# Performance work log

Measured on AMD Instinct MI355X. Metric: run time of the kernel, lower is better.

Reference implementation:

```python
import jax, jax.numpy as jnp
import numpy as np
import math

T, R, H, DK = 3, 4, 8, 32   # num_types, num_relations, n_heads, d_k
OUT = H * DK                # out_dim = 256
IN = 256                    # in_dim (== out_dim, required by residual)
B, N = 4, 1024              # batch, max_nodes
LN_EPS = 1e-5


def setup_inputs() -> dict:
    key = jax.random.key(0)
    ks = jax.random.split(key, 12)
    a = math.sqrt(6.0 / (2 * DK))  # xavier_uniform bound for [d_k,d_k]
    w = 0.02
    return {
        "node_features":   jax.random.normal(ks[0], (B, N, IN), jnp.float32),
        "node_types_soft": jax.random.uniform(ks[1], (B, N, T), jnp.float32),
        "adj_matrix_soft": jax.random.uniform(ks[2], (B, N, N), jnp.float32),
        "edge_types_soft": jax.random.uniform(ks[3], (B, N, N, R), jnp.float32),
        "Wq": jax.random.normal(ks[4], (T, IN, OUT), jnp.float32) * w,
        "bq": jnp.zeros((T, OUT), jnp.float32),
        "Wk": jax.random.normal(ks[5], (T, IN, OUT), jnp.float32) * w,
        "bk": jnp.zeros((T, OUT), jnp.float32),
        "Wv": jax.random.normal(ks[6], (T, IN, OUT), jnp.float32) * w,
        "bv": jnp.zeros((T, OUT), jnp.float32),
        "Wa": jax.random.normal(ks[7], (T, OUT, OUT), jnp.float32) * w,
        "ba": jnp.zeros((T, OUT), jnp.float32),
        "rel_pri": jnp.ones((R, H), jnp.float32),
        "rel_att": jax.random.uniform(ks[8], (R, H, DK, DK), jnp.float32, -a, a),
        "rel_msg": jax.random.uniform(ks[9], (R, H, DK, DK), jnp.float32, -a, a),
        "skip": jnp.ones((T,), jnp.float32),
        "ln_gamma": jnp.ones((T, OUT), jnp.float32),
        "ln_beta": jnp.zeros((T, OUT), jnp.float32),
    }


def _single(x, types, adj, erel, Wq, bq, Wk, bk, Wv, bv, Wa, ba,
            rel_pri, rel_att, rel_msg, skip, ln_gamma, ln_beta):
    # x:[N,in], types:[N,T], adj:[N,N], erel:[N,N,R]
    n = x.shape[0]
    sqrt_dk = float(np.sqrt(DK))
    # per-type projections -> [T,N,H,DK]
    Qt = (jnp.einsum('nd,tdo->tno', x, Wq) + bq[:, None, :]).reshape(T, n, H, DK)
    Kt = (jnp.einsum('nd,tdo->tno', x, Wk) + bk[:, None, :]).reshape(T, n, H, DK)
    Vt = (jnp.einsum('nd,tdo->tno', x, Wv) + bv[:, None, :]).reshape(T, n, H, DK)
    # relation-transformed K/V: [T,R,N,H,DK]
    Ksr = jnp.einsum('tnhd,rhde->trnhe', Kt, rel_att)
    Vsr = jnp.einsum('tnhd,rhde->trnhe', Vt, rel_msg)
    # soft-type mixtures (sums over target/source types factor out of the mask)
    Qbar = jnp.einsum('nt,tnhd->nhd', types, Qt)            # target mix
    Kbar = jnp.einsum('nt,trnhd->rnhd', types, Ksr)         # source mix, per relation
    # accumulated (masked, unnormalized) attention logits [N,N,H]
    res_att = jnp.zeros((n, n, H), x.dtype)
    for r in range(R):
        coef = (adj * erel[:, :, r])[:, :, None] * (rel_pri[r] / sqrt_dk)  # [N,N,H]
        res_att = res_att + coef * jnp.einsum('ihd,jhd->ijh', Qbar, Kbar[r])
    # per-target-row softmax over sources (dim j), zeroed if row-sum tiny
    row_sum = res_att.sum(axis=(1, 2))                       # [N]
    attn = jnp.where((row_sum > 1e-6)[:, None, None],
                     jax.nn.softmax(res_att, axis=1), 0.0)
    # aggregated = sum_{s,r,j} attn * masked score * V_{s,r}  (never builds [N,N,H,DK])
    agg = jnp.zeros((n, H, DK), x.dtype)
    for r in range(R):
        coef = (adj * erel[:, :, r])[:, :, None] * (rel_pri[r] / sqrt_dk)
        for s in range(T):
            score = coef * types[None, :, s, None] * jnp.einsum('ihd,jhd->ijh', Qbar, Ksr[s, r])
            agg = agg + jnp.einsum('ijh,ijh,jhd->ihd', attn, score, Vsr[s, r])
    agg = agg.reshape(n, OUT)
    # per-type output head: a_linear(gelu(agg)), gated residual, layernorm, soft-type mix
    g = jax.nn.gelu(agg, approximate=False)
    trans = jnp.einsum('no,tod->tnd', g, Wa) + ba[:, None, :]          # [T,N,OUT]
    alpha = jax.nn.sigmoid(skip)[:, None, None]
    res = trans * alpha + x[None] * (1.0 - alpha)
    mu = res.mean(axis=-1, keepdims=True)
    var = ((res - mu) ** 2).mean(axis=-1, keepdims=True)
    ln = (res - mu) / jnp.sqrt(var + LN_EPS) * ln_gamma[:, None, :] + ln_beta[:, None, :]
    return jnp.einsum('nt,tnd->nd', types, ln)


def reference(node_features, node_types_soft, adj_matrix_soft, edge_types_soft,
              Wq, bq, Wk, bk, Wv, bv, Wa, ba, rel_pri, rel_att, rel_msg,
              skip, ln_gamma, ln_beta):
    f = jax.vmap(_single, in_axes=(0, 0, 0, 0) + (None,) * 14)
    return f(node_features, node_types_soft, adj_matrix_soft, edge_types_soft,
             Wq, bq, Wk, bk, Wv, bv, Wa, ba, rel_pri, rel_att, rel_msg,
             skip, ln_gamma, ln_beta)
```

## Files before the change

kernel.cpp:

```cpp
#include <hip/hip_runtime.h>
#include <math.h>

constexpr int CB = 4, CN = 1024, CT = 3, CR = 4, CH = 8, CDK = 32, COUT = 256;

typedef __attribute__((ext_vector_type(4))) float f32x4;
typedef __attribute__((ext_vector_type(8))) short s16x8;
typedef __attribute__((ext_vector_type(4))) _Float16 f16x4;
typedef __attribute__((ext_vector_type(8))) _Float16 f16x8;
typedef __attribute__((ext_vector_type(4))) unsigned short u16x4;
typedef __attribute__((ext_vector_type(8))) unsigned short u16x8;

__device__ inline unsigned short f2bf(float x) {
    unsigned u = __float_as_uint(x);
    unsigned r = (u + 0x7fffu + ((u >> 16) & 1u)) >> 16;
    return (unsigned short)r;
}
__device__ inline float bf2f(unsigned short b) {
    return __uint_as_float(((unsigned)b) << 16);
}

__global__ void zero_rs(float* __restrict__ rs) {
    rs[blockIdx.x * 256 + threadIdx.x] = 0.f;
}

__global__ void splitx(const float* __restrict__ X,
                       unsigned short* __restrict__ Xh, unsigned short* __restrict__ Xl)
{
    size_t idx = ((size_t)blockIdx.x * 256 + threadIdx.x) * 4;
    f32x4 v = *(const f32x4*)(X + idx);
    u16x4 hv, lv;
    #pragma unroll
    for (int k = 0; k < 4; ++k) {
        unsigned short hb = f2bf(v[k]);
        hv[k] = hb;
        lv[k] = f2bf(v[k] - bf2f(hb));
    }
    *(u16x4*)(Xh + idx) = hv;
    *(u16x4*)(Xl + idx) = lv;
}

__global__ __launch_bounds__(256) void wsplit(
    const float* __restrict__ Wq, const float* __restrict__ Wk,
    const float* __restrict__ Wv, const float* __restrict__ Wa,
    unsigned short* __restrict__ WTh, unsigned short* __restrict__ WTl)
{
    int z = blockIdx.z;
    int t = z % 3;
    const float* W;
    if (z < 9) { int w3 = z / 3; W = (w3 == 0 ? Wq : (w3 == 1 ? Wk : Wv)); }
    else W = Wa;
    W += (size_t)t * COUT * COUT;
    int k0 = blockIdx.x * 32, n0 = blockIdx.y * 32;
    __shared__ float tl[32][33];
    int tid = threadIdx.x;
    {
        int k = tid >> 3, n4 = (tid & 7) * 4;
        f32x4 v = *(const f32x4*)(W + (size_t)(k0 + k) * COUT + n0 + n4);
        tl[n4 + 0][k] = v[0]; tl[n4 + 1][k] = v[1];
        tl[n4 + 2][k] = v[2]; tl[n4 + 3][k] = v[3];
    }
    __syncthreads();
    int n = tid >> 3, k4 = (tid & 7) * 4;
    u16x4 hv, lv;
    #pragma unroll
    for (int j = 0; j < 4; ++j) {
        float x = tl[n][k4 + j];
        unsigned short hb = f2bf(x);
        hv[j] = hb; lv[j] = f2bf(x - bf2f(hb));
    }
    size_t off = (size_t)z * COUT * COUT + (size_t)(n0 + n) * COUT + k0 + k4;
    *(u16x4*)(WTh + off) = hv;
    *(u16x4*)(WTl + off) = lv;
}

__global__ __launch_bounds__(256) void mfma_gemm(
    int mode,
    const unsigned short* __restrict__ Ah, const unsigned short* __restrict__ Al,
    const unsigned short* __restrict__ WTh, const unsigned short* __restrict__ WTl,
    const float* __restrict__ bq, const float* __restrict__ bk,
    const float* __restrict__ bv, const float* __restrict__ ba,
    float* __restrict__ Y0, float* __restrict__ Y1, float* __restrict__ Y2)
{
    int z = blockIdx.z;
    int b, t, widx;
    const float* bias;
    float* Y;
    if (mode == 0) {
        b = z / 9; int r9 = z % 9; int w3 = r9 / 3; t = r9 % 3;
        widx = w3 * 3 + t;
        bias = (w3 == 0 ? bq : (w3 == 1 ? bk : bv)) + t * COUT;
        Y = (w3 == 0 ? Y0 : (w3 == 1 ? Y1 : Y2)) + ((size_t)b * CT + t) * CN * COUT;
    } else {
        b = z / CT; t = z % CT;
        widx = 9 + t;
        bias = ba + t * COUT;
        Y = Y0 + ((size_t)b * CT + t) * CN * COUT;
    }
    const unsigned short* Ahb = Ah + (size_t)b * CN * COUT;
    const unsigned short* Alb = Al + (size_t)b * CN * COUT;
    const unsigned short* Bhb = WTh + (size_t)widx * COUT * COUT;
    const unsigned short* Blb = WTl + (size_t)widx * COUT * COUT;

    const int M0 = blockIdx.x * 128, N0 = blockIdx.y * 128;
    __shared__ unsigned short As[2][128][40];
    __shared__ unsigned short Bs[2][128][40];
    const int tid = threadIdx.x;
    const int wave = tid >> 6, lane = tid & 63;
    const int wm = wave & 1, wn = wave >> 1;
    const int col = lane & 15, quad = lane >> 4;

    f32x4 acc[4][4];
    #pragma unroll
    for (int mt = 0; mt < 4; ++mt)
        #pragma unroll
        for (int nt = 0; nt < 4; ++nt) acc[mt][nt] = (f32x4){0.f, 0.f, 0.f, 0.f};

    for (int kt = 0; kt < COUT; kt += 32) {
        #pragma unroll
        for (int q = 0; q < 2; ++q) {
            int f = q * 256 + tid;
            int m = f >> 2, kc = (f & 3) * 8;
            *(u16x8*)&As[0][m][kc] = *(const u16x8*)(Ahb + (size_t)(M0 + m) * COUT + kt + kc);
            *(u16x8*)&As[1][m][kc] = *(const u16x8*)(Alb + (size_t)(M0 + m) * COUT + kt + kc);
            *(u16x8*)&Bs[0][m][kc] = *(const u16x8*)(Bhb + (size_t)(N0 + m) * COUT + kt + kc);
            *(u16x8*)&Bs[1][m][kc] = *(const u16x8*)(Blb + (size_t)(N0 + m) * COUT + kt + kc);
        }
        __syncthreads();
        s16x8 ah[4], al4[4], bh[4], bl4[4];
        #pragma unroll
        for (int mt = 0; mt < 4; ++mt) {
            ah[mt]  = *(const s16x8*)&As[0][wm * 64 + mt * 16 + col][quad * 8];
            al4[mt] = *(const s16x8*)&As[1][wm * 64 + mt * 16 + col][quad * 8];
        }
        #pragma unroll
        for (int nt = 0; nt < 4; ++nt) {
            bh[nt]  = *(const s16x8*)&Bs[0][wn * 64 + nt * 16 + col][quad * 8];
            bl4[nt] = *(const s16x8*)&Bs[1][wn * 64 + nt * 16 + col][quad * 8];
        }
        #pragma unroll
        for (int mt = 0; mt < 4; ++mt)
            #pragma unroll
            for (int nt = 0; nt < 4; ++nt) {
                acc[mt][nt] = __builtin_amdgcn_mfma_f32_16x16x32_bf16(al4[mt], bh[nt], acc[mt][nt], 0, 0, 0);
                acc[mt][nt] = __builtin_amdgcn_mfma_f32_16x16x32_bf16(ah[mt], bl4[nt], acc[mt][nt], 0, 0, 0);
                acc[mt][nt] = __builtin_amdgcn_mfma_f32_16x16x32_bf16(ah[mt], bh[nt], acc[mt][nt], 0, 0, 0);
            }
        __syncthreads();
    }
    float bb[4];
    #pragma unroll
    for (int nt = 0; nt < 4; ++nt) bb[nt] = bias[N0 + wn * 64 + nt * 16 + col];
    #pragma unroll
    for (int mt = 0; mt < 4; ++mt)
        #pragma unroll
        for (int nt = 0; nt < 4; ++nt) {
            int n = N0 + wn * 64 + nt * 16 + col;
            #pragma unroll
            for (int reg = 0; reg < 4; ++reg) {
                int m = M0 + wm * 64 + mt * 16 + quad * 4 + reg;
                Y[(size_t)m * COUT + n] = acc[mt][nt][reg] + bb[nt];
            }
        }
}

__global__ void mix_qbar(const float* __restrict__ Qt, const float* __restrict__ types,
                         float* __restrict__ Qbar)
{
    int idx = blockIdx.x * 256 + threadIdx.x;
    int bi = idx >> 6;
    int o4 = (idx & 63) * 4;
    int b = bi >> 10;
    const float* tp = types + (size_t)bi * CT;
    float t0 = tp[0], t1 = tp[1], t2 = tp[2];
    size_t nbase = ((size_t)b * CT) * CN * COUT + (size_t)(bi & 1023) * COUT + o4;
    float4 q0 = *(const float4*)(Qt + nbase);
    float4 q1 = *(const float4*)(Qt + nbase + (size_t)CN * COUT);
    float4 q2 = *(const float4*)(Qt + nbase + 2 * (size_t)CN * COUT);
    float4 o;
    o.x = t0 * q0.x + t1 * q1.x + t2 * q2.x;
    o.y = t0 * q0.y + t1 * q1.y + t2 * q2.y;
    o.z = t0 * q0.z + t1 * q1.z + t2 * q2.z;
    o.w = t0 * q0.w + t1 * q1.w + t2 * q2.w;
    *(float4*)(Qbar + (size_t)bi * COUT + o4) = o;
}

__global__ __launch_bounds__(256) void qr3_kernel(const float* __restrict__ Qbar,
                                                  const float* __restrict__ rel_att,
                                                  const float* __restrict__ rel_pri,
                                                  unsigned short* __restrict__ Qrhi,
                                                  unsigned short* __restrict__ Qrlo)
{
    int i0 = blockIdx.x * 8;
    int rh = blockIdx.y; int r = rh >> 3, h = rh & 7;
    int b = blockIdx.z;
    __shared__ float A_s[32][33];
    __shared__ float q_s[8][32];
    int tid = threadIdx.x;
    {
        int f = tid * 4; int d = f >> 5, e = f & 31;
        float4 v = *(const float4*)(rel_att + ((size_t)rh * 32 + d) * 32 + e);
        A_s[d][e] = v.x; A_s[d][e + 1] = v.y; A_s[d][e + 2] = v.z; A_s[d][e + 3] = v.w;
        int ii = tid >> 5, ee = tid & 31;
        q_s[ii][ee] = Qbar[((size_t)b * CN + i0 + ii) * COUT + h * CDK + ee];
    }
    __syncthreads();
    int d = tid & 31, ii = tid >> 5;
    float acc = 0.f;
    #pragma unroll 8
    for (int e = 0; e < 32; ++e) acc += A_s[d][e] * q_s[ii][e];
    const float inv_sqrt = 0.17677669529663687f;
    float v = acc * rel_pri[rh] * inv_sqrt;
    unsigned short hb = f2bf(v);
    float lo = v - bf2f(hb);
    size_t oidx = ((((size_t)b * CR + r) * CH + h) * CN + i0 + ii) * CDK + d;
    Qrhi[oidx] = hb;
    Qrlo[oidx] = f2bf(lo);
}

__global__ __launch_bounds__(256) void prep_k(const float* __restrict__ Kt,
                                              const float* __restrict__ types,
                                              unsigned short* __restrict__ Kbh,
                                              unsigned short* __restrict__ Kbl,
                                              unsigned short* __restrict__ Kty)
{
    int b = blockIdx.y;
    int j = blockIdx.x * 8 + (threadIdx.x >> 5);
    int c = threadIdx.x & 31;
    int h = c >> 2, d0 = (c & 3) * 8;
    const float* tp = types + ((size_t)b * CN + j) * CT;
    float kb[8];
    #pragma unroll
    for (int k = 0; k < 8; ++k) kb[k] = 0.f;
    #pragma unroll
    for (int s = 0; s < 3; ++s) {
        float ty = tp[s];
        const float* src = Kt + (((size_t)(b * 3 + s)) * CN + j) * COUT + c * 8;
        f32x4 a0 = *(const f32x4*)(src);
        f32x4 a1 = *(const f32x4*)(src + 4);
        u16x8 kt8;
        #pragma unroll
        for (int k = 0; k < 4; ++k) {
            float v0 = ty * a0[k], v1 = ty * a1[k];
            kt8[k] = f2bf(v0); kt8[4 + k] = f2bf(v1);
            kb[k] += v0; kb[4 + k] += v1;
        }
        *(u16x8*)(Kty + (((size_t)(b * 3 + s) * CH + h) * CN + j) * CDK + d0) = kt8;
    }
    u16x8 hv, lv;
    #pragma unroll
    for (int k = 0; k < 8; ++k) {
        unsigned short hb = f2bf(kb[k]);
        hv[k] = hb; lv[k] = f2bf(kb[k] - bf2f(hb));
    }
    *(u16x8*)(Kbh + (((size_t)b * CH + h) * CN + j) * CDK + d0) = hv;
    *(u16x8*)(Kbl + (((size_t)b * CH + h) * CN + j) * CDK + d0) = lv;
}

__global__ __launch_bounds__(256) void vT_kernel(const float* __restrict__ Vt,
                                                 _Float16* __restrict__ VT)
{
    int j0 = blockIdx.x * 64; int h = blockIdx.y; int bs = blockIdx.z;
    __shared__ float tile[32][72];
    int t = threadIdx.x;
    int jj = t >> 2, e8 = (t & 3) * 8;
    const float* src = Vt + ((size_t)bs * CN + j0 + jj) * COUT + h * CDK + e8;
    f32x4 v0 = *(const f32x4*)(src);
    f32x4 v1 = *(const f32x4*)(src + 4);
    #pragma unroll
    for (int k = 0; k < 4; ++k) { tile[e8 + k][jj] = v0[k]; tile[e8 + 4 + k][jj] = v1[k]; }
    __syncthreads();
    int e = t >> 3, jr = (t & 7) * 8;
    f16x8 o;
    #pragma unroll
    for (int k = 0; k < 8; ++k) o[k] = (_Float16)tile[e][jr + k];
    *(f16x8*)(VT + (((size_t)bs * CH + h) * CDK + e) * CN + j0 + jr) = o;
}

__global__ void mT_kernel(const float* __restrict__ rel_msg, _Float16* __restrict__ MT)
{
    int rh = blockIdx.x; int t = threadIdx.x;
    int e = t >> 3, ep4 = (t & 7) * 4;
    f16x4 o;
    #pragma unroll
    for (int k = 0; k < 4; ++k)
        o[k] = (_Float16)rel_msg[((size_t)rh * 32 + ep4 + k) * 32 + e];
    *(f16x4*)(MT + ((size_t)rh * 32 + e) * 32 + ep4) = o;
}

__global__ __launch_bounds__(256) void coef_t(const float* __restrict__ adj,
                                              const float* __restrict__ erel,
                                              float* __restrict__ coefT)
{
    int b = blockIdx.z; int i0 = blockIdx.y * 32; int j0 = blockIdx.x * 32;
    __shared__ float tile[32][132];
    int t = threadIdx.x;
    {
        int ii = t >> 3, jc = t & 7;
        size_t arow = ((size_t)b * CN + i0 + ii) * CN + j0;
        f32x4 av = *(const f32x4*)(adj + arow + jc * 4);
        #pragma unroll
        for (int kk = 0; kk < 4; ++kk) {
            int j = jc * 4 + kk;
            f32x4 ev = *(const f32x4*)(erel + (arow + j) * 4);
            float a = av[kk];
            f32x4 cv;
            cv[0] = ev[0] * a; cv[1] = ev[1] * a; cv[2] = ev[2] * a; cv[3] = ev[3] * a;
            *(f32x4*)&tile[j][ii * 4] = cv;
        }
    }
    __syncthreads();
    {
        int jj = t >> 3, ic = t & 7;
        size_t orow = ((size_t)b * CN + j0 + jj) * CN + i0;
        #pragma unroll
        for (int kk = 0; kk < 4; ++kk)
            *(f32x4*)(coefT + (orow + ic * 4 + kk) * 4) = *(const f32x4*)&tile[jj][(ic * 4 + kk) * 4];
    }
}

__global__ __launch_bounds__(256, 3) void attn3_kernel(
    const unsigned short* __restrict__ Qrhi, const unsigned short* __restrict__ Qrlo,
    const unsigned short* __restrict__ Kbh,  const unsigned short* __restrict__ Kbl,
    const unsigned short* __restrict__ Kty,
    const _Float16* __restrict__ VT,
    const float* __restrict__ coefT,
    float* __restrict__ Upart,
    float* __restrict__ lbuf,
    float* __restrict__ rowsum)
{
    const int h = blockIdx.y;
    const int z = blockIdx.z; const int b = z >> 1, part = z & 1;
    const int tid = threadIdx.x;
    const int wave = tid >> 6, lane = tid & 63;
    const int col = lane & 15, quad = lane >> 4;
    const int i = blockIdx.x * 64 + wave * 16 + col;
    const int jbase = part * 512;

    __shared__ _Float16 vs[2][3][32][20];

    s16x8 qh[4], ql[4];
    #pragma unroll
    for (int r = 0; r < 4; ++r) {
        size_t off = ((((size_t)b * CR + r) * CH + h) * CN + i) * CDK + quad * 8;
        qh[r] = *(const s16x8*)(Qrhi + off);
        ql[r] = *(const s16x8*)(Qrlo + off);
    }

    const int e_st = tid >> 3, jc_st = tid & 7;
    size_t vtb[3];
    #pragma unroll
    for (int s = 0; s < 3; ++s)
        vtb[s] = (((size_t)(b * 3 + s) * CH + h) * CDK + e_st) * CN + jc_st * 2;

    #pragma unroll
    for (int s = 0; s < 3; ++s)
        *(unsigned*)&vs[0][s][e_st][jc_st * 2] = *(const unsigned*)(VT + vtb[s] + jbase);
    __syncthreads();

    f32x4 U[4][2];
    #pragma unroll
    for (int r = 0; r < 4; ++r) { U[r][0] = (f32x4){0.f,0.f,0.f,0.f}; U[r][1] = (f32x4){0.f,0.f,0.f,0.f}; }
    float lpart = 0.f, rspart = 0.f;

    const size_t kbbase = (((size_t)b * CH + h) * CN + col) * CDK + quad * 8;
    size_t ktbase[3];
    #pragma unroll
    for (int s = 0; s < 3; ++s)
        ktbase[s] = (((size_t)(b * 3 + s) * CH + h) * CN + col) * CDK + quad * 8;

    #pragma unroll 1
    for (int js = 0; js < 32; ++js) {
        const int j0 = jbase + js * 16;
        const int buf = js & 1;
        const int jn = jbase + ((js + 1 < 32) ? (js + 1) * 16 : js * 16);
        unsigned pf0 = *(const unsigned*)(VT + vtb[0] + jn);
        unsigned pf1 = *(const unsigned*)(VT + vtb[1] + jn);
        unsigned pf2 = *(const unsigned*)(VT + vtb[2] + jn);

        s16x8 kbh_ = *(const s16x8*)(Kbh + kbbase + (size_t)j0 * CDK);
        s16x8 kbl_ = *(const s16x8*)(Kbl + kbbase + (size_t)j0 * CDK);
        s16x8 kt[3];
        #pragma unroll
        for (int s = 0; s < 3; ++s)
            kt[s] = *(const s16x8*)(Kty + ktbase[s] + (size_t)j0 * CDK);
        f32x4 cf[4];
        #pragma unroll
        for (int reg = 0; reg < 4; ++reg)
            cf[reg] = *(const f32x4*)(coefT + (((size_t)b * CN + j0 + quad * 4 + reg) * CN + i) * 4);

        f32x4 Db[4];
        #pragma unroll
        for (int r = 0; r < 4; ++r) {
            f32x4 d = {0.f, 0.f, 0.f, 0.f};
            d = __builtin_amdgcn_mfma_f32_16x16x32_bf16(kbl_, qh[r], d, 0, 0, 0);
            d = __builtin_amdgcn_mfma_f32_16x16x32_bf16(kbh_, ql[r], d, 0, 0, 0);
            d = __builtin_amdgcn_mfma_f32_16x16x32_bf16(kbh_, qh[r], d, 0, 0, 0);
            Db[r] = d;
        }
        float P[4];
        #pragma unroll
        for (int reg = 0; reg < 4; ++reg) {
            float L = cf[reg][0] * Db[0][reg] + cf[reg][1] * Db[1][reg]
                    + cf[reg][2] * Db[2][reg] + cf[reg][3] * Db[3][reg];
            rspart += L;
            P[reg] = __expf(L);
            lpart += P[reg];
        }
        #pragma unroll
        for (int s = 0; s < 3; ++s) {
            f32x4 Dp[4];
            #pragma unroll
            for (int r = 0; r < 4; ++r) {
                f32x4 d = {0.f, 0.f, 0.f, 0.f};
                Dp[r] = __builtin_amdgcn_mfma_f32_16x16x32_bf16(kt[s], qh[r], d, 0, 0, 0);
            }
            f16x4 v0 = *(const f16x4*)&vs[buf][s][col][quad * 4];
            f16x4 v1 = *(const f16x4*)&vs[buf][s][col + 16][quad * 4];
            #pragma unroll
            for (int r = 0; r < 4; ++r) {
                f16x4 w;
                w[0] = (_Float16)(P[0] * cf[0][r] * Dp[r][0]);
                w[1] = (_Float16)(P[1] * cf[1][r] * Dp[r][1]);
                w[2] = (_Float16)(P[2] * cf[2][r] * Dp[r][2]);
                w[3] = (_Float16)(P[3] * cf[3][r] * Dp[r][3]);
                U[r][0] = __builtin_amdgcn_mfma_f32_16x16x16f16(v0, w, U[r][0], 0, 0, 0);
                U[r][1] = __builtin_amdgcn_mfma_f32_16x16x16f16(v1, w, U[r][1], 0, 0, 0);
            }
        }
        *(unsigned*)&vs[buf ^ 1][0][e_st][jc_st * 2] = pf0;
        *(unsigned*)&vs[buf ^ 1][1][e_st][jc_st * 2] = pf1;
        *(unsigned*)&vs[buf ^ 1][2][e_st][jc_st * 2] = pf2;
        __syncthreads();
    }

    float l = lpart;  l += __shfl_xor(l, 16);  l += __shfl_xor(l, 32);
    float rv = rspart; rv += __shfl_xor(rv, 16); rv += __shfl_xor(rv, 32);
    if (quad == 0) {
        lbuf[(((size_t)part * CB + b) * CH + h) * CN + i] = l;
        atomicAdd(rowsum + (size_t)b * CN + i, rv);
    }
    int itile = blockIdx.x * 4 + wave;
    size_t ub = ((((size_t)(b * CH + h) * 64 + itile) * 2 + part)) * 2048;
    #pragma unroll
    for (int r = 0; r < 4; ++r)
        #pragma unroll
        for (int eh = 0; eh < 2; ++eh)
            *(f32x4*)(Upart + ub + (size_t)(r * 2 + eh) * 256 + lane * 4) = U[r][eh];
}

__global__ __launch_bounds__(256) void merge_gelu(
    const float* __restrict__ Upart, const float* __restrict__ lbuf,
    const _Float16* __restrict__ MT, const float* __restrict__ rowsum,
    unsigned short* __restrict__ Gh, unsigned short* __restrict__ Gl)
{
    const int h = blockIdx.y, b = blockIdx.z;
    const int tid = threadIdx.x;
    const int wave = tid >> 6, lane = tid & 63;
    const int col = lane & 15, quad = lane >> 4;
    const int itile = blockIdx.x * 4 + wave;
    const int i = itile * 16 + col;

    size_t ub = ((size_t)(b * CH + h) * 64 + itile) * 2 * 2048;
    f32x4 U[4][2];
    #pragma unroll
    for (int r = 0; r < 4; ++r)
        #pragma unroll
        for (int eh = 0; eh < 2; ++eh) {
            f32x4 a = *(const f32x4*)(Upart + ub + (size_t)(r * 2 + eh) * 256 + lane * 4);
            f32x4 c = *(const f32x4*)(Upart + ub + 2048 + (size_t)(r * 2 + eh) * 256 + lane * 4);
            U[r][eh] = a + c;
        }
    float l = lbuf[(((size_t)0 * CB + b) * CH + h) * CN + i]
            + lbuf[(((size_t)1 * CB + b) * CH + h) * CN + i];
    float il = 1.f / l;
    f16x4 Uh[4][2];
    #pragma unroll
    for (int r = 0; r < 4; ++r)
        #pragma unroll
        for (int eh = 0; eh < 2; ++eh) {
            Uh[r][eh][0] = (_Float16)(U[r][eh][0] * il);
            Uh[r][eh][1] = (_Float16)(U[r][eh][1] * il);
            Uh[r][eh][2] = (_Float16)(U[r][eh][2] * il);
            Uh[r][eh][3] = (_Float16)(U[r][eh][3] * il);
        }
    float rsv = rowsum[(size_t)b * CN + i];
    bool gate = rsv > 1e-6f;
    const float is2 = 0.70710678118654752f;
    #pragma unroll
    for (int eo = 0; eo < 2; ++eo) {
        f32x4 acc = {0.f, 0.f, 0.f, 0.f};
        #pragma unroll
        for (int r = 0; r < 4; ++r)
            #pragma unroll
            for (int ep = 0; ep < 2; ++ep) {
                f16x4 mt = *(const f16x4*)(MT + ((size_t)(r * 8 + h) * 32 + eo * 16 + col) * 32
                                               + ep * 16 + quad * 4);
                acc = __builtin_amdgcn_mfma_f32_16x16x16f16(mt, Uh[r][ep], acc, 0, 0, 0);
            }
        u16x4 hv, lv;
        #pragma unroll
        for (int k = 0; k < 4; ++k) {
            float x = gate ? acc[k] : 0.f;
            float g = 0.5f * x * (1.f + erff(x * is2));
            unsigned short hb = f2bf(g);
            hv[k] = hb; lv[k] = f2bf(g - bf2f(hb));
        }
        size_t off = ((size_t)b * CN + i) * COUT + h * CDK + eo * 16 + quad * 4;
        *(u16x4*)(Gh + off) = hv;
        *(u16x4*)(Gl + off) = lv;
    }
}

__global__ __launch_bounds__(256) void final_ln2(
    const float* __restrict__ trans, const float* __restrict__ x,
    const float* __restrict__ types, const float* __restrict__ skip,
    const float* __restrict__ gamma, const float* __restrict__ beta,
    float* __restrict__ out)
{
    int wave = threadIdx.x >> 6, lane = threadIdx.x & 63;
    int bi = blockIdx.x * 4 + wave;
    int b = bi >> 10, i = bi & 1023;
    f32x4 xo = *(const f32x4*)(x + (size_t)bi * COUT + lane * 4);
    f32x4 accum = {0.f, 0.f, 0.f, 0.f};
    const float* tp = types + (size_t)bi * CT;
    #pragma unroll 1
    for (int t = 0; t < CT; ++t) {
        float al = 1.f / (1.f + __expf(-skip[t]));
        f32x4 tr = *(const f32x4*)(trans + (((size_t)b * CT + t) * CN + i) * COUT + lane * 4);
        f32x4 res;
        float s = 0.f;
        #pragma unroll
        for (int k = 0; k < 4; ++k) { res[k] = tr[k] * al + xo[k] * (1.f - al); s += res[k]; }
        #pragma unroll
        for (int mk = 1; mk < 64; mk <<= 1) s += __shfl_xor(s, mk);
        float mu = s * (1.f / COUT);
        f32x4 dc; float s2 = 0.f;
        #pragma unroll
        for (int k = 0; k < 4; ++k) { dc[k] = res[k] - mu; s2 += dc[k] * dc[k]; }
        #pragma unroll
        for (int mk = 1; mk < 64; mk <<= 1) s2 += __shfl_xor(s2, mk);
        float inv = rsqrtf(s2 * (1.f / COUT) + 1e-5f);
        f32x4 g = *(const f32x4*)(gamma + (size_t)t * COUT + lane * 4);
        f32x4 be = *(const f32x4*)(beta + (size_t)t * COUT + lane * 4);
        float ty = tp[t];
        #pragma unroll
        for (int k = 0; k < 4; ++k) accum[k] += ty * (dc[k] * inv * g[k] + be[k]);
    }
    *(f32x4*)(out + (size_t)bi * COUT + lane * 4) = accum;
}

extern "C" void kernel_launch(void* const* d_in, const int* in_sizes, int n_in,
                              void* d_out, int out_size, void* d_ws, size_t ws_size,
                              hipStream_t stream)
{
    (void)in_sizes; (void)n_in; (void)out_size; (void)ws_size;
    const float* nf      = (const float*)d_in[0];
    const float* types   = (const float*)d_in[1];
    const float* adj     = (const float*)d_in[2];
    const float* erel    = (const float*)d_in[3];
    const float* Wq      = (const float*)d_in[4];
    const float* bq      = (const float*)d_in[5];
    const float* Wk      = (const float*)d_in[6];
    const float* bk      = (const float*)d_in[7];
    const float* Wv      = (const float*)d_in[8];
    const float* bv      = (const float*)d_in[9];
    const float* Wa      = (const float*)d_in[10];
    const float* ba      = (const float*)d_in[11];
    const float* rel_pri = (const float*)d_in[12];
    const float* rel_att = (const float*)d_in[13];
    const float* rel_msg = (const float*)d_in[14];
    const float* skip    = (const float*)d_in[15];
    const float* gamma   = (const float*)d_in[16];
    const float* beta    = (const float*)d_in[17];
    float* out = (float*)d_out;

    float* ws = (float*)d_ws;
    size_t o = 0;
    float* pool0 = ws + o; o += 3 * (size_t)CB * CT * CN * COUT;
    float* Qt  = pool0;
    float* Ktb = pool0 + (size_t)CB * CT * CN * COUT;
    float* Vtb = pool0 + 2 * (size_t)CB * CT * CN * COUT;
    float* Qbar = ws + o; o += (size_t)CB * CN * COUT;
    float* rsb  = ws + o; o += (size_t)CB * CN;
    float* lbufp = ws + o; o += 2 * (size_t)CB * CH * CN;
    unsigned short* Qrhi = (unsigned short*)(ws + o); o += (size_t)CB * CR * CN * COUT / 2;
    unsigned short* Qrlo = (unsigned short*)(ws + o); o += (size_t)CB * CR * CN * COUT / 2;
    unsigned short* Kbh  = (unsigned short*)(ws + o); o += (size_t)CB * CH * CN * CDK / 2;
    unsigned short* Kbl  = (unsigned short*)(ws + o); o += (size_t)CB * CH * CN * CDK / 2;
    unsigned short* Kty  = (unsigned short*)(ws + o); o += (size_t)CB * CT * CH * CN * CDK / 2;
    _Float16* VTb = (_Float16*)(ws + o);              o += (size_t)CB * CT * CH * CDK * CN / 2;
    _Float16* MTb = (_Float16*)(ws + o);              o += (size_t)CR * CH * CDK * CDK / 2;
    unsigned short* Xh = (unsigned short*)(ws + o);   o += (size_t)CB * CN * COUT / 2;
    unsigned short* Xl = (unsigned short*)(ws + o);   o += (size_t)CB * CN * COUT / 2;
    unsigned short* Gh = (unsigned short*)(ws + o);   o += (size_t)CB * CN * COUT / 2;
    unsigned short* Gl = (unsigned short*)(ws + o);   o += (size_t)CB * CN * COUT / 2;
    unsigned short* WTh = (unsigned short*)(ws + o);  o += (size_t)12 * COUT * COUT / 2;
    unsigned short* WTl = (unsigned short*)(ws + o);  o += (size_t)12 * COUT * COUT / 2;
    float* coefT = ws + o; o += (size_t)CB * CN * CN * CR;
    float* Upart  = pool0;
    float* transb = pool0 + 3 * (size_t)CB * CN * COUT;

    zero_rs<<<CB * CN / 256, 256, 0, stream>>>(rsb);
    splitx<<<CB * CN * COUT / 4 / 256, 256, 0, stream>>>(nf, Xh, Xl);
    wsplit<<<dim3(8, 8, 12), 256, 0, stream>>>(Wq, Wk, Wv, Wa, WTh, WTl);
    mfma_gemm<<<dim3(8, 2, CB * 9), 256, 0, stream>>>(0, Xh, Xl, WTh, WTl,
                                                      bq, bk, bv, ba, Qt, Ktb, Vtb);
    coef_t<<<dim3(32, 32, CB), 256, 0, stream>>>(adj, erel, coefT);
    mix_qbar<<<CB * CN * COUT / 4 / 256, 256, 0, stream>>>(Qt, types, Qbar);
    qr3_kernel<<<dim3(CN / 8, CR * CH, CB), 256, 0, stream>>>(Qbar, rel_att, rel_pri, Qrhi, Qrlo);
    prep_k<<<dim3(CN / 8, CB), 256, 0, stream>>>(Ktb, types, Kbh, Kbl, Kty);
    vT_kernel<<<dim3(CN / 64, CH, CB * CT), 256, 0, stream>>>(Vtb, VTb);
    mT_kernel<<<CR * CH, 256, 0, stream>>>(rel_msg, MTb);
    attn3_kernel<<<dim3(16, CH, CB * 2), 256, 0, stream>>>(Qrhi, Qrlo, Kbh, Kbl, Kty, VTb, coefT,
                                                           Upart, lbufp, rsb);
    merge_gelu<<<dim3(16, CH, CB), 256, 0, stream>>>(Upart, lbufp, MTb, rsb, Gh, Gl);
    mfma_gemm<<<dim3(8, 2, CB * CT), 256, 0, stream>>>(1, Gh, Gl, WTh, WTl,
                                                       bq, bk, bv, ba, transb, transb, transb);
    final_ln2<<<CB * CN / 4, 256, 0, stream>>>(transb, nf, types, skip, gamma, beta, out);
}
```

Measured before the change: 383.1 us.

## Merge prep kernels into fewer launches and prefetch K/coef in attention loop

Result: faster. 374.7 us (-2.2%).

```diff
diff --git a/kernel.cpp b/kernel.cpp
--- a/kernel.cpp
+++ b/kernel.cpp
@@ -5,11 +5,14 @@
 
 typedef __attribute__((ext_vector_type(4))) float f32x4;
 typedef __attribute__((ext_vector_type(8))) short s16x8;
+typedef __attribute__((ext_vector_type(2))) _Float16 f16x2;
 typedef __attribute__((ext_vector_type(4))) _Float16 f16x4;
 typedef __attribute__((ext_vector_type(8))) _Float16 f16x8;
 typedef __attribute__((ext_vector_type(4))) unsigned short u16x4;
 typedef __attribute__((ext_vector_type(8))) unsigned short u16x8;
 
+union W4 { f16x4 v4; f16x2 v2[2]; };
+
 __device__ inline unsigned short f2bf(float x) {
     unsigned u = __float_as_uint(x);
     unsigned r = (u + 0x7fffu + ((u >> 16) & 1u)) >> 16;
@@ -18,59 +21,102 @@
 __device__ inline float bf2f(unsigned short b) {
     return __uint_as_float(((unsigned)b) << 16);
 }
-
-__global__ void zero_rs(float* __restrict__ rs) {
-    rs[blockIdx.x * 256 + threadIdx.x] = 0.f;
-}
-
-__global__ void splitx(const float* __restrict__ X,
-                       unsigned short* __restrict__ Xh, unsigned short* __restrict__ Xl)
-{
-    size_t idx = ((size_t)blockIdx.x * 256 + threadIdx.x) * 4;
-    f32x4 v = *(const f32x4*)(X + idx);
-    u16x4 hv, lv;
-    #pragma unroll
-    for (int k = 0; k < 4; ++k) {
-        unsigned short hb = f2bf(v[k]);
-        hv[k] = hb;
-        lv[k] = f2bf(v[k] - bf2f(hb));
-    }
-    *(u16x4*)(Xh + idx) = hv;
-    *(u16x4*)(Xl + idx) = lv;
-}
-
-__global__ __launch_bounds__(256) void wsplit(
+__device__ inline f16x2 pk2(float a, float b) {
+    auto t = __builtin_amdgcn_cvt_pkrtz(a, b);
+    f16x2 r;
+    __builtin_memcpy(&r, &t, sizeof(r));
+    return r;
+}
+
+__global__ __launch_bounds__(256) void prep0(
+    const float* __restrict__ nf,
+    unsigned short* __restrict__ Xh, unsigned short* __restrict__ Xl,
     const float* __restrict__ Wq, const float* __restrict__ Wk,
     const float* __restrict__ Wv, const float* __restrict__ Wa,
-    unsigned short* __restrict__ WTh, unsigned short* __restrict__ WTl)
-{
-    int z = blockIdx.z;
-    int t = z % 3;
-    const float* W;
-    if (z < 9) { int w3 = z / 3; W = (w3 == 0 ? Wq : (w3 == 1 ? Wk : Wv)); }
-    else W = Wa;
-    W += (size_t)t * COUT * COUT;
-    int k0 = blockIdx.x * 32, n0 = blockIdx.y * 32;
-    __shared__ float tl[32][33];
-    int tid = threadIdx.x;
-    {
-        int k = tid >> 3, n4 = (tid & 7) * 4;
-        f32x4 v = *(const f32x4*)(W + (size_t)(k0 + k) * COUT + n0 + n4);
-        tl[n4 + 0][k] = v[0]; tl[n4 + 1][k] = v[1];
-        tl[n4 + 2][k] = v[2]; tl[n4 + 3][k] = v[3];
-    }
-    __syncthreads();
-    int n = tid >> 3, k4 = (tid & 7) * 4;
-    u16x4 hv, lv;
-    #pragma unroll
-    for (int j = 0; j < 4; ++j) {
-        float x = tl[n][k4 + j];
-        unsigned short hb = f2bf(x);
-        hv[j] = hb; lv[j] = f2bf(x - bf2f(hb));
-    }
-    size_t off = (size_t)z * COUT * COUT + (size_t)(n0 + n) * COUT + k0 + k4;
-    *(u16x4*)(WTh + off) = hv;
-    *(u16x4*)(WTl + off) = lv;
+    unsigned short* __restrict__ WTh, unsigned short* __restrict__ WTl,
+    const float* __restrict__ rel_msg, _Float16* __restrict__ MT,
+    float* __restrict__ rs,
+    const float* __restrict__ adj, const float* __restrict__ erel,
+    float* __restrict__ coefT)
+{
+    __shared__ float smem[32 * 132];
+    const int bx = blockIdx.x, tid = threadIdx.x;
+    if (bx < 1024) {
+        size_t idx = ((size_t)bx * 256 + tid) * 4;
+        f32x4 v = *(const f32x4*)(nf + idx);
+        u16x4 hv, lv;
+        #pragma unroll
+        for (int k = 0; k < 4; ++k) {
+            unsigned short hb = f2bf(v[k]);
+            hv[k] = hb; lv[k] = f2bf(v[k] - bf2f(hb));
+        }
+        *(u16x4*)(Xh + idx) = hv;
+        *(u16x4*)(Xl + idx) = lv;
+    } else if (bx < 1792) {
+        int w = bx - 1024;
+        int zz = w >> 6; int rem = w & 63;
+        int k0 = (rem >> 3) * 32, n0 = (rem & 7) * 32;
+        int t = zz % 3;
+        const float* W;
+        if (zz < 9) { int w3 = zz / 3; W = (w3 == 0 ? Wq : (w3 == 1 ? Wk : Wv)); }
+        else W = Wa;
+        W += (size_t)t * COUT * COUT;
+        {
+            int k = tid >> 3, n4 = (tid & 7) * 4;
+            f32x4 v = *(const f32x4*)(W + (size_t)(k0 + k) * COUT + n0 + n4);
+            smem[(n4 + 0) * 33 + k] = v[0]; smem[(n4 + 1) * 33 + k] = v[1];
+            smem[(n4 + 2) * 33 + k] = v[2]; smem[(n4 + 3) * 33 + k] = v[3];
+        }
+        __syncthreads();
+        int n = tid >> 3, k4 = (tid & 7) * 4;
+        u16x4 hv, lv;
+        #pragma unroll
+        for (int j = 0; j < 4; ++j) {
+            float x = smem[n * 33 + k4 + j];
+            unsigned short hb = f2bf(x);
+            hv[j] = hb; lv[j] = f2bf(x - bf2f(hb));
+        }
+        size_t off = (size_t)zz * COUT * COUT + (size_t)(n0 + n) * COUT + k0 + k4;
+        *(u16x4*)(WTh + off) = hv;
+        *(u16x4*)(WTl + off) = lv;
+    } else if (bx < 1824) {
+        int rh = bx - 1792;
+        int e = tid >> 3, ep4 = (tid & 7) * 4;
+        f16x4 o;
+        #pragma unroll
+        for (int k = 0; k < 4; ++k)
+            o[k] = (_Float16)rel_msg[((size_t)rh * 32 + ep4 + k) * 32 + e];
+        *(f16x4*)(MT + ((size_t)rh * 32 + e) * 32 + ep4) = o;
+    } else if (bx < 1840) {
+        rs[(bx - 1824) * 256 + tid] = 0.f;
+    } else {
+        int c = bx - 1840;
+        int b = c >> 10; int rem = c & 1023;
+        int i0 = (rem >> 5) * 32; int j0 = (rem & 31) * 32;
+        {
+            int ii = tid >> 3, jc = tid & 7;
+            size_t arow = ((size_t)b * CN + i0 + ii) * CN + j0;
+            f32x4 av = *(const f32x4*)(adj + arow + jc * 4);
+            #pragma unroll
+            for (int kk = 0; kk < 4; ++kk) {
+                int j = jc * 4 + kk;
+                f32x4 ev = *(const f32x4*)(erel + (arow + j) * 4);
+                float a = av[kk];
+                f32x4 cv;
+                cv[0] = ev[0] * a; cv[1] = ev[1] * a; cv[2] = ev[2] * a; cv[3] = ev[3] * a;
+                *(f32x4*)&smem[j * 132 + ii * 4] = cv;
+            }
+        }
+        __syncthreads();
+        {
+            int jj = tid >> 3, ic = tid & 7;
+            size_t orow = ((size_t)b * CN + j0 + jj) * CN + i0;
+            #pragma unroll
+            for (int kk = 0; kk < 4; ++kk)
+                *(f32x4*)(coefT + (orow + ic * 4 + kk) * 4) =
+                    *(const f32x4*)&smem[jj * 132 + (ic * 4 + kk) * 4];
+        }
+    }
 }
 
 __global__ __launch_bounds__(256) void mfma_gemm(
@@ -217,116 +263,72 @@
     Qrlo[oidx] = f2bf(lo);
 }
 
-__global__ __launch_bounds__(256) void prep_k(const float* __restrict__ Kt,
-                                              const float* __restrict__ types,
-                                              unsigned short* __restrict__ Kbh,
-                                              unsigned short* __restrict__ Kbl,
-                                              unsigned short* __restrict__ Kty)
-{
-    int b = blockIdx.y;
-    int j = blockIdx.x * 8 + (threadIdx.x >> 5);
-    int c = threadIdx.x & 31;
-    int h = c >> 2, d0 = (c & 3) * 8;
-    const float* tp = types + ((size_t)b * CN + j) * CT;
-    float kb[8];
-    #pragma unroll
-    for (int k = 0; k < 8; ++k) kb[k] = 0.f;
-    #pragma unroll
-    for (int s = 0; s < 3; ++s) {
-        float ty = tp[s];
-        const float* src = Kt + (((size_t)(b * 3 + s)) * CN + j) * COUT + c * 8;
-        f32x4 a0 = *(const f32x4*)(src);
-        f32x4 a1 = *(const f32x4*)(src + 4);
-        u16x8 kt8;
-        #pragma unroll
-        for (int k = 0; k < 4; ++k) {
-            float v0 = ty * a0[k], v1 = ty * a1[k];
-            kt8[k] = f2bf(v0); kt8[4 + k] = f2bf(v1);
-            kb[k] += v0; kb[4 + k] += v1;
-        }
-        *(u16x8*)(Kty + (((size_t)(b * 3 + s) * CH + h) * CN + j) * CDK + d0) = kt8;
-    }
-    u16x8 hv, lv;
-    #pragma unroll
-    for (int k = 0; k < 8; ++k) {
-        unsigned short hb = f2bf(kb[k]);
-        hv[k] = hb; lv[k] = f2bf(kb[k] - bf2f(hb));
-    }
-    *(u16x8*)(Kbh + (((size_t)b * CH + h) * CN + j) * CDK + d0) = hv;
-    *(u16x8*)(Kbl + (((size_t)b * CH + h) * CN + j) * CDK + d0) = lv;
-}
-
-__global__ __launch_bounds__(256) void vT_kernel(const float* __restrict__ Vt,
-                                                 _Float16* __restrict__ VT)
-{
-    int j0 = blockIdx.x * 64; int h = blockIdx.y; int bs = blockIdx.z;
+__global__ __launch_bounds__(256) void prep_kv(
+    const float* __restrict__ Kt, const float* __restrict__ Vt,
+    const float* __restrict__ types,
+    unsigned short* __restrict__ Kbh, unsigned short* __restrict__ Kbl,
+    unsigned short* __restrict__ Kty, _Float16* __restrict__ VT)
+{
     __shared__ float tile[32][72];
-    int t = threadIdx.x;
-    int jj = t >> 2, e8 = (t & 3) * 8;
-    const float* src = Vt + ((size_t)bs * CN + j0 + jj) * COUT + h * CDK + e8;
-    f32x4 v0 = *(const f32x4*)(src);
-    f32x4 v1 = *(const f32x4*)(src + 4);
-    #pragma unroll
-    for (int k = 0; k < 4; ++k) { tile[e8 + k][jj] = v0[k]; tile[e8 + 4 + k][jj] = v1[k]; }
-    __syncthreads();
-    int e = t >> 3, jr = (t & 7) * 8;
-    f16x8 o;
-    #pragma unroll
-    for (int k = 0; k < 8; ++k) o[k] = (_Float16)tile[e][jr + k];
-    *(f16x8*)(VT + (((size_t)bs * CH + h) * CDK + e) * CN + j0 + jr) = o;
-}
-
-__global__ void mT_kernel(const float* __restrict__ rel_msg, _Float16* __restrict__ MT)
-{
-    int rh = blockIdx.x; int t = threadIdx.x;
-    int e = t >> 3, ep4 = (t & 7) * 4;
-    f16x4 o;
-    #pragma unroll
-    for (int k = 0; k < 4; ++k)
-        o[k] = (_Float16)rel_msg[((size_t)rh * 32 + ep4 + k) * 32 + e];
-    *(f16x4*)(MT + ((size_t)rh * 32 + e) * 32 + ep4) = o;
-}
-
-__global__ __launch_bounds__(256) void coef_t(const float* __restrict__ adj,
-                                              const float* __restrict__ erel,
-                                              float* __restrict__ coefT)
-{
-    int b = blockIdx.z; int i0 = blockIdx.y * 32; int j0 = blockIdx.x * 32;
-    __shared__ float tile[32][132];
-    int t = threadIdx.x;
-    {
-        int ii = t >> 3, jc = t & 7;
-        size_t arow = ((size_t)b * CN + i0 + ii) * CN + j0;
-        f32x4 av = *(const f32x4*)(adj + arow + jc * 4);
-        #pragma unroll
-        for (int kk = 0; kk < 4; ++kk) {
-            int j = jc * 4 + kk;
-            f32x4 ev = *(const f32x4*)(erel + (arow + j) * 4);
-            float a = av[kk];
-            f32x4 cv;
-            cv[0] = ev[0] * a; cv[1] = ev[1] * a; cv[2] = ev[2] * a; cv[3] = ev[3] * a;
-            *(f32x4*)&tile[j][ii * 4] = cv;
-        }
-    }
-    __syncthreads();
-    {
-        int jj = t >> 3, ic = t & 7;
-        size_t orow = ((size_t)b * CN + j0 + jj) * CN + i0;
-        #pragma unroll
-        for (int kk = 0; kk < 4; ++kk)
-            *(f32x4*)(coefT + (orow + ic * 4 + kk) * 4) = *(const f32x4*)&tile[jj][(ic * 4 + kk) * 4];
-    }
-}
-
-__global__ __launch_bounds__(256, 3) void attn3_kernel(
+    const int bx = blockIdx.x, tid = threadIdx.x;
+    if (bx < 512) {
+        int b = bx >> 7, jt = bx & 127;
+        int j = jt * 8 + (tid >> 5);
+        int c = tid & 31;
+        int h = c >> 2, d0 = (c & 3) * 8;
+        const float* tp = types + ((size_t)b * CN + j) * CT;
+        float kb[8];
+        #pragma unroll
+        for (int k = 0; k < 8; ++k) kb[k] = 0.f;
+        #pragma unroll
+        for (int s = 0; s < 3; ++s) {
+            float ty = tp[s];
+            const float* src = Kt + (((size_t)(b * 3 + s)) * CN + j) * COUT + c * 8;
+            f32x4 a0 = *(const f32x4*)(src);
+            f32x4 a1 = *(const f32x4*)(src + 4);
+            u16x8 kt8;
+            #pragma unroll
+            for (int k = 0; k < 4; ++k) {
+                float v0 = ty * a0[k], v1 = ty * a1[k];
+                kt8[k] = f2bf(v0); kt8[4 + k] = f2bf(v1);
+                kb[k] += v0; kb[4 + k] += v1;
+            }
+            *(u16x8*)(Kty + (((size_t)(b * 3 + s) * CH + h) * CN + j) * CDK + d0) = kt8;
+        }
+        u16x8 hv, lv;
+        #pragma unroll
+        for (int k = 0; k < 8; ++k) {
+            unsigned short hb = f2bf(kb[k]);
+            hv[k] = hb; lv[k] = f2bf(kb[k] - bf2f(hb));
+        }
+        *(u16x8*)(Kbh + (((size_t)b * CH + h) * CN + j) * CDK + d0) = hv;
+        *(u16x8*)(Kbl + (((size_t)b * CH + h) * CN + j) * CDK + d0) = lv;
+    } else {
+        int idx2 = bx - 512;
+        int bs = idx2 >> 7; int rem = idx2 & 127;
+        int h = rem >> 4; int j0 = (rem & 15) * 64;
+        int jj = tid >> 2, e8 = (tid & 3) * 8;
+        const float* src = Vt + ((size_t)bs * CN + j0 + jj) * COUT + h * CDK + e8;
+        f32x4 v0 = *(const f32x4*)(src);
+        f32x4 v1 = *(const f32x4*)(src + 4);
+        #pragma unroll
+        for (int k = 0; k < 4; ++k) { tile[e8 + k][jj] = v0[k]; tile[e8 + 4 + k][jj] = v1[k]; }
+        __syncthreads();
+        int e = tid >> 3, jr = (tid & 7) * 8;
+        f16x8 o;
+        #pragma unroll
+        for (int k = 0; k < 8; ++k) o[k] = (_Float16)tile[e][jr + k];
+        *(f16x8*)(VT + (((size_t)bs * CH + h) * CDK + e) * CN + j0 + jr) = o;
+    }
+}
+
+__global__ __launch_bounds__(256, 3) void attn4_kernel(
     const unsigned short* __restrict__ Qrhi, const unsigned short* __restrict__ Qrlo,
     const unsigned short* __restrict__ Kbh,  const unsigned short* __restrict__ Kbl,
     const unsigned short* __restrict__ Kty,
     const _Float16* __restrict__ VT,
     const float* __restrict__ coefT,
-    float* __restrict__ Upart,
-    float* __restrict__ lbuf,
-    float* __restrict__ rowsum)
+    float* __restrict__ Upart, float* __restrict__ lbuf, float* __restrict__ rowsum)
 {
     const int h = blockIdx.y;
     const int z = blockIdx.z; const int b = z >> 1, part = z & 1;
@@ -355,7 +357,6 @@
     #pragma unroll
     for (int s = 0; s < 3; ++s)
         *(unsigned*)&vs[0][s][e_st][jc_st * 2] = *(const unsigned*)(VT + vtb[s] + jbase);
-    __syncthreads();
 
     f32x4 U[4][2];
     #pragma unroll
@@ -367,64 +368,80 @@
     #pragma unroll
     for (int s = 0; s < 3; ++s)
         ktbase[s] = (((size_t)(b * 3 + s) * CH + h) * CN + col) * CDK + quad * 8;
-
-    #pragma unroll 1
+    const size_t cfrow = ((size_t)b * CN + quad * 4) * CN + i;
+
+    s16x8 p_bh[2], p_bl[2];
+    f32x4 p_cf[2][4];
+    {
+        const int j0 = jbase;
+        p_bh[0] = *(const s16x8*)(Kbh + kbbase + (size_t)j0 * CDK);
+        p_bl[0] = *(const s16x8*)(Kbl + kbbase + (size_t)j0 * CDK);
+        #pragma unroll
+        for (int reg = 0; reg < 4; ++reg)
+            p_cf[0][reg] = *(const f32x4*)(coefT + (cfrow + (size_t)(j0 + reg) * CN) * 4);
+    }
+    __syncthreads();
+
+    #pragma unroll 2
     for (int js = 0; js < 32; ++js) {
+        const int cur = js & 1, nx = cur ^ 1;
         const int j0 = jbase + js * 16;
         const int buf = js & 1;
+        s16x8 kt0 = *(const s16x8*)(Kty + ktbase[0] + (size_t)j0 * CDK);
+        s16x8 kt1 = *(const s16x8*)(Kty + ktbase[1] + (size_t)j0 * CDK);
+        s16x8 kt2 = *(const s16x8*)(Kty + ktbase[2] + (size_t)j0 * CDK);
         const int jn = jbase + ((js + 1 < 32) ? (js + 1) * 16 : js * 16);
         unsigned pf0 = *(const unsigned*)(VT + vtb[0] + jn);
         unsigned pf1 = *(const unsigned*)(VT + vtb[1] + jn);
         unsigned pf2 = *(const unsigned*)(VT + vtb[2] + jn);
-
-        s16x8 kbh_ = *(const s16x8*)(Kbh + kbbase + (size_t)j0 * CDK);
-        s16x8 kbl_ = *(const s16x8*)(Kbl + kbbase + (size_t)j0 * CDK);
-        s16x8 kt[3];
-        #pragma unroll
-        for (int s = 0; s < 3; ++s)
-            kt[s] = *(const s16x8*)(Kty + ktbase[s] + (size_t)j0 * CDK);
-        f32x4 cf[4];
+        p_bh[nx] = *(const s16x8*)(Kbh + kbbase + (size_t)jn * CDK);
+        p_bl[nx] = *(const s16x8*)(Kbl + kbbase + (size_t)jn * CDK);
         #pragma unroll
         for (int reg = 0; reg < 4; ++reg)
-            cf[reg] = *(const f32x4*)(coefT + (((size_t)b * CN + j0 + quad * 4 + reg) * CN + i) * 4);
+            p_cf[nx][reg] = *(const f32x4*)(coefT + (cfrow + (size_t)(jn + reg) * CN) * 4);
 
         f32x4 Db[4];
         #pragma unroll
         for (int r = 0; r < 4; ++r) {
             f32x4 d = {0.f, 0.f, 0.f, 0.f};
-            d = __builtin_amdgcn_mfma_f32_16x16x32_bf16(kbl_, qh[r], d, 0, 0, 0);
-            d = __builtin_amdgcn_mfma_f32_16x16x32_bf16(kbh_, ql[r], d, 0, 0, 0);
-            d = __builtin_amdgcn_mfma_f32_16x16x32_bf16(kbh_, qh[r], d, 0, 0, 0);
+            d = __builtin_amdgcn_mfma_f32_16x16x32_bf16(p_bl[cur], qh[r], d, 0, 0, 0);
+            d = __builtin_amdgcn_mfma_f32_16x16x32_bf16(p_bh[cur], ql[r], d, 0, 0, 0);
+            d = __builtin_amdgcn_mfma_f32_16x16x32_bf16(p_bh[cur], qh[r], d, 0, 0, 0);
             Db[r] = d;
         }
         float P[4];
         #pragma unroll
         for (int reg = 0; reg < 4; ++reg) {
-            float L = cf[reg][0] * Db[0][reg] + cf[reg][1] * Db[1][reg]
-                    + cf[reg][2] * Db[2][reg] + cf[reg][3] * Db[3][reg];
+            float L = p_cf[cur][reg][0] * Db[0][reg] + p_cf[cur][reg][1] * Db[1][reg]
+                    + p_cf[cur][reg][2] * Db[2][reg] + p_cf[cur][reg][3] * Db[3][reg];
             rspart += L;
             P[reg] = __expf(L);
             lpart += P[reg];
         }
+        f16x2 pA[4], pB[4];
+        #pragma unroll
+        for (int r = 0; r < 4; ++r) {
+            pA[r] = pk2(P[0] * p_cf[cur][0][r], P[1] * p_cf[cur][1][r]);
+            pB[r] = pk2(P[2] * p_cf[cur][2][r], P[3] * p_cf[cur][3][r]);
+        }
         #pragma unroll
         for (int s = 0; s < 3; ++s) {
+            s16x8 kts = (s == 0) ? kt0 : (s == 1) ? kt1 : kt2;
             f32x4 Dp[4];
             #pragma unroll
             for (int r = 0; r < 4; ++r) {
                 f32x4 d = {0.f, 0.f, 0.f, 0.f};
-                Dp[r] = __builtin_amdgcn_mfma_f32_16x16x32_bf16(kt[s], qh[r], d, 0, 0, 0);
+                Dp[r] = __builtin_amdgcn_mfma_f32_16x16x32_bf16(kts, qh[r], d, 0, 0, 0);
             }
             f16x4 v0 = *(const f16x4*)&vs[buf][s][col][quad * 4];
             f16x4 v1 = *(const f16x4*)&vs[buf][s][col + 16][quad * 4];
             #pragma unroll
             for (int r = 0; r < 4; ++r) {
-                f16x4 w;
-                w[0] = (_Float16)(P[0] * cf[0][r] * Dp[r][0]);
-                w[1] = (_Float16)(P[1] * cf[1][r] * Dp[r][1]);
-                w[2] = (_Float16)(P[2] * cf[2][r] * Dp[r][2]);
-                w[3] = (_Float16)(P[3] * cf[3][r] * Dp[r][3]);
-                U[r][0] = __builtin_amdgcn_mfma_f32_16x16x16f16(v0, w, U[r][0], 0, 0, 0);
-                U[r][1] = __builtin_amdgcn_mfma_f32_16x16x16f16(v1, w, U[r][1], 0, 0, 0);
+                W4 w;
+                w.v2[0] = pA[r] * pk2(Dp[r][0], Dp[r][1]);
+                w.v2[1] = pB[r] * pk2(Dp[r][2], Dp[r][3]);
+                U[r][0] = __builtin_amdgcn_mfma_f32_16x16x16f16(v0, w.v4, U[r][0], 0, 0, 0);
+                U[r][1] = __builtin_amdgcn_mfma_f32_16x16x16f16(v1, w.v4, U[r][1], 0, 0, 0);
             }
         }
         *(unsigned*)&vs[buf ^ 1][0][e_st][jc_st * 2] = pf0;
@@ -600,18 +617,14 @@
     float* Upart  = pool0;
     float* transb = pool0 + 3 * (size_t)CB * CN * COUT;
 
-    zero_rs<<<CB * CN / 256, 256, 0, stream>>>(rsb);
-    splitx<<<CB * CN * COUT / 4 / 256, 256, 0, stream>>>(nf, Xh, Xl);
-    wsplit<<<dim3(8, 8, 12), 256, 0, stream>>>(Wq, Wk, Wv, Wa, WTh, WTl);
+    prep0<<<5936, 256, 0, stream>>>(nf, Xh, Xl, Wq, Wk, Wv, Wa, WTh, WTl,
+                                    rel_msg, MTb, rsb, adj, erel, coefT);
     mfma_gemm<<<dim3(8, 2, CB * 9), 256, 0, stream>>>(0, Xh, Xl, WTh, WTl,
                                                       bq, bk, bv, ba, Qt, Ktb, Vtb);
-    coef_t<<<dim3(32, 32, CB), 256, 0, stream>>>(adj, erel, coefT);
     mix_qbar<<<CB * CN * COUT / 4 / 256, 256, 0, stream>>>(Qt, types, Qbar);
     qr3_kernel<<<dim3(CN / 8, CR * CH, CB), 256, 0, stream>>>(Qbar, rel_att, rel_pri, Qrhi, Qrlo);
-    prep_k<<<dim3(CN / 8, CB), 256, 0, stream>>>(Ktb, types, Kbh, Kbl, Kty);
-    vT_kernel<<<dim3(CN / 64, CH, CB * CT), 256, 0, stream>>>(Vtb, VTb);
-    mT_kernel<<<CR * CH, 256, 0, stream>>>(rel_msg, MTb);
-    attn3_kernel<<<dim3(16, CH, CB * 2), 256, 0, stream>>>(Qrhi, Qrlo, Kbh, Kbl, Kty, VTb, coefT,
+    prep_kv<<<2048, 256, 0, stream>>>(Ktb, Vtb, types, Kbh, Kbl, Kty, VTb);
+    attn4_kernel<<<dim3(16, CH, CB * 2), 256, 0, stream>>>(Qrhi, Qrlo, Kbh, Kbl, Kty, VTb, coefT,
                                                            Upart, lbufp, rsb);
     merge_gelu<<<dim3(16, CH, CB), 256, 0, stream>>>(Upart, lbufp, MTb, rsb, Gh, Gl);
     mfma_gemm<<<dim3(8, 2, CB * CT), 256, 0, stream>>>(1, Gh, Gl, WTh, WTl,
```
